# Kernel optimization log

Hardware: AMD Instinct MI355X
Metric: run time of the kernel (lower is better)

The kernel has to match this reference:

```python
import jax, jax.numpy as jnp
import numpy as np

ALPHA = 1.0          # gating temperature (train_alpha=False)
DEPTH = 4            # floor(log2(leaves=16))
LEAF_NUM = 16        # 2**DEPTH
N_INTERNAL = LEAF_NUM - 2  # nodes 1..14 (root handled separately)
B, D, OUT = 8192, 512, 64


def _prob(x, pw, aW, ab):
    # vectorized Node.prob with set_comps=True (comparators recomputed from batch mean)
    comp = -jnp.mean(x * pw, axis=0)                      # [in]
    dist = jax.nn.sigmoid(ALPHA * (pw * x + comp))        # [B, in]
    attn = jax.nn.softmax(x @ aW.T + ab, axis=-1)         # [B, in]
    return jnp.sum(dist * attn, axis=1, keepdims=True)    # [B, 1]


def setup_inputs() -> dict:
    key = jax.random.key(0)
    ks = jax.random.split(key, 12)
    s = 0.02
    return {
        "x": jax.random.normal(ks[0], (B, D), jnp.float32),
        # root node (input_size=D, output_size=D)
        "calc_W0": jax.random.normal(ks[1], (D, D), jnp.float32) * s,
        "calc_b0": jnp.zeros((D,), jnp.float32),
        "prob_w0": jax.random.uniform(ks[2], (D,), jnp.float32),
        "attn_W0": jax.random.normal(ks[3], (D, D), jnp.float32) * s,
        "attn_b0": jnp.zeros((D,), jnp.float32),
        # internal nodes 1..14 (input_size=2D, output_size=D), stacked
        "calc_W": jax.random.normal(ks[4], (N_INTERNAL, D, 2 * D), jnp.float32) * s,
        "calc_b": jnp.zeros((N_INTERNAL, D), jnp.float32),
        "prob_w": jax.random.uniform(ks[5], (N_INTERNAL, 2 * D), jnp.float32),
        "attn_W": jax.random.normal(ks[6], (N_INTERNAL, 2 * D, 2 * D), jnp.float32) * s,
        "attn_b": jnp.zeros((N_INTERNAL, 2 * D), jnp.float32),
        # leaf nodes: learned output vectors (torch.rand init)
        "leaf_out": jax.random.uniform(ks[7], (LEAF_NUM, OUT), jnp.float32),
    }


def reference(x, calc_W0, calc_b0, prob_w0, attn_W0, attn_b0,
              calc_W, calc_b, prob_w, attn_W, attn_b, leaf_out):
    outs, probab = {}, {}
    # root
    outs[0] = jax.nn.relu(x @ calc_W0.T + calc_b0)            # [B, D]
    p = _prob(x, prob_w0, attn_W0, attn_b0)                   # [B, 1]
    probab[1] = 1.0 - p
    probab[2] = p
    # internal nodes 1..leaf_num-2 (binary-tree routing)
    for n in range(1, LEAF_NUM - 1):
        parent = (n - 1) // 2
        inp = jnp.concatenate([outs[parent], x], axis=1)      # [B, 2D]
        outs[n] = jax.nn.relu(inp @ calc_W[n - 1].T + calc_b[n - 1])
        p = _prob(inp, prob_w[n - 1], attn_W[n - 1], attn_b[n - 1])
        probab[2 * n + 1] = probab[n] * (1.0 - p)
        probab[2 * n + 2] = probab[n] * p
    # leaves: indices LEAF_NUM-1 .. 2*LEAF_NUM-2
    leaf_p = jnp.concatenate([probab[i + LEAF_NUM - 1] for i in range(LEAF_NUM)], axis=1)  # [B, 16]
    # sum over leaves of probab * leaf_out == leaf_p @ leaf_out
    actions = leaf_p @ leaf_out                                # [B, OUT]
    return jax.nn.softmax(actions, axis=-1)
```

## Files before the change

### kernel.cpp

```cpp
#include <hip/hip_runtime.h>
#include <hip/hip_bf16.h>
#include <cstdint>


#define NROWS 8192
#define HALFD 512

typedef __bf16 bf16x8 __attribute__((ext_vector_type(8)));
typedef short  short8 __attribute__((ext_vector_type(8)));
typedef float  f32x4  __attribute__((ext_vector_type(4)));

union FragU { short8 s; bf16x8 b; };

struct GArgs {
  const __hip_bfloat16* A0[4];
  const __hip_bfloat16* Bw[4];
  const float* bias[4];
  const float* pw[4];
  const float* cm0[4];
  __hip_bfloat16* outB[4];
  float* csOut[4];
  float* S1[4];
  float* S2[4];
  int mode[4];
  int gx[4];
  int K[4];
};

__device__ __forceinline__ void gl2lds16(const void* g, void* l) {
  __builtin_amdgcn_global_load_lds((__attribute__((address_space(1))) void*)g,
                                   (__attribute__((address_space(3))) void*)l,
                                   16, 0, 0);
}

struct CvtArgs { const float* src[5]; __hip_bfloat16* dst[5]; int nblk[5]; };
__global__ void k_cvt(CvtArgs a) {
  int b = blockIdx.x, r = 0;
  while (b >= a.nblk[r]) { b -= a.nblk[r]; ++r; }
  const int i = (b * 256 + threadIdx.x) * 4;
  float4 v = *(const float4*)(a.src[r] + i);
  union { short4 s4; __hip_bfloat16 h[4]; } u;
  u.h[0] = __float2bfloat16(v.x);
  u.h[1] = __float2bfloat16(v.y);
  u.h[2] = __float2bfloat16(v.z);
  u.h[3] = __float2bfloat16(v.w);
  *(short4*)(a.dst[r] + i) = u.s4;
}

__global__ void k_colsum_f32(const float* __restrict__ src, float* __restrict__ dst) {
  int c  = blockIdx.x * 256 + threadIdx.x;
  int r0 = blockIdx.y * 256;
  float s = 0.f;
  for (int r = 0; r < 256; ++r) s += src[(size_t)(r0 + r) * HALFD + c];
  atomicAdd(&dst[c], s);
}

__global__ __launch_bounds__(512, 2)
void k_gemm(GArgs ga, const __hip_bfloat16* __restrict__ A1,
            const float* __restrict__ cm1) {
  __shared__ alignas(16) short As[2][256 * 64];
  __shared__ alignas(16) short Bs[2][256 * 64];

  const int z = blockIdx.z;
  const int id  = blockIdx.x + gridDim.x * blockIdx.y;
  const int xcd = id & 7;
  const int q   = id >> 3;
  const int bx  = q >> 2;
  const int by  = xcd * 4 + (q & 3);
  if (bx >= ga.gx[z]) return;

  const __hip_bfloat16* __restrict__ Ah0 = ga.A0[z];
  const __hip_bfloat16* __restrict__ Bw  = ga.Bw[z];
  const float* __restrict__ bias = ga.bias[z];
  const int K = ga.K[z];

  const int tid  = threadIdx.x;
  const int lane = tid & 63;
  const int wv   = tid >> 6;
  const int wm   = wv >> 2, wn = wv & 3;
  const int lr   = lane & 15, lg = lane >> 4;
  const int sw   = lr & 7;
  const int row0 = by * 256;
  const int col0 = bx * 256;

  f32x4 acc[8][4];
#pragma unroll
  for (int i = 0; i < 8; ++i)
#pragma unroll
    for (int j = 0; j < 4; ++j)
#pragma unroll
      for (int e = 0; e < 4; ++e) acc[i][j][e] = 0.f;

  const int sr  = tid >> 3;
  const int sc  = (((tid & 7) ^ (sr & 7)) << 3);
  const int wvB = wv * 1024;

#pragma unroll
  for (int rnd = 0; rnd < 4; ++rnd) {
    const int r = rnd * 64 + sr;
    gl2lds16(Ah0 + (size_t)(row0 + r) * HALFD + sc, (char*)As[0] + rnd * 8192 + wvB);
    gl2lds16(Bw  + (size_t)(col0 + r) * K + sc,     (char*)Bs[0] + rnd * 8192 + wvB);
  }
  __syncthreads();

  int cur = 0;
  for (int kt = 0; kt < K; kt += 64) {
    const int kn = kt + 64;
    if (kn < K) {
      const __hip_bfloat16* Asrc = (kn < HALFD) ? Ah0 : A1;
      const int kl = kn & (HALFD - 1);
#pragma unroll
      for (int rnd = 0; rnd < 4; ++rnd) {
        const int r = rnd * 64 + sr;
        gl2lds16(Asrc + (size_t)(row0 + r) * HALFD + kl + sc,
                 (char*)As[cur ^ 1] + rnd * 8192 + wvB);
        gl2lds16(Bw + (size_t)(col0 + r) * K + kn + sc,
                 (char*)Bs[cur ^ 1] + rnd * 8192 + wvB);
      }
    }
    const short* Ab = As[cur];
    const short* Bb = Bs[cur];
#pragma unroll
    for (int kk = 0; kk < 64; kk += 32) {
      FragU a[8], b[4];
#pragma unroll
      for (int mi = 0; mi < 8; ++mi)
        a[mi].s = *(const short8*)(Ab + (wm * 128 + mi * 16 + lr) * 64 +
                                   ((((kk >> 3) + lg) ^ sw) << 3));
#pragma unroll
      for (int ni = 0; ni < 4; ++ni)
        b[ni].s = *(const short8*)(Bb + (wn * 64 + ni * 16 + lr) * 64 +
                                   ((((kk >> 3) + lg) ^ sw) << 3));
#pragma unroll
      for (int mi = 0; mi < 8; ++mi)
#pragma unroll
        for (int ni = 0; ni < 4; ++ni)
          acc[mi][ni] = __builtin_amdgcn_mfma_f32_16x16x32_bf16(a[mi].b, b[ni].b,
                                                               acc[mi][ni], 0, 0, 0);
    }
    __syncthreads();
    cur ^= 1;
  }

  if (ga.mode[z] == 0) {
    __hip_bfloat16* outB = ga.outB[z];
    float* csOut = ga.csOut[z];
#pragma unroll
    for (int ni = 0; ni < 4; ++ni) {
      const int col  = col0 + wn * 64 + ni * 16 + lr;
      const float bv = bias[col];
      __hip_bfloat16* op = outB + (size_t)(col >> 9) * ((size_t)NROWS * HALFD) + (col & 511);
      float csum = 0.f;
#pragma unroll
      for (int mi = 0; mi < 8; ++mi) {
#pragma unroll
        for (int rg = 0; rg < 4; ++rg) {
          const int row = row0 + wm * 128 + mi * 16 + lg * 4 + rg;
          float v = acc[mi][ni][rg] + bv;
          v = v > 0.f ? v : 0.f;
          csum += v;
          op[(size_t)row * HALFD] = __float2bfloat16(v);
        }
      }
      csum += __shfl_xor(csum, 16);
      csum += __shfl_xor(csum, 32);
      if (lg == 0) atomicAdd(&csOut[col], csum);
    }
  } else {
    const float* __restrict__ pw  = ga.pw[z];
    const float* __restrict__ cm0 = ga.cm0[z];
    const int node  = col0 >> 10;
    const int slice = ((bx & 3) << 2) | wn;
    float* s1p = ga.S1[z] + (size_t)(node * 16 + slice) * NROWS;
    float* s2p = ga.S2[z] + (size_t)(node * 16 + slice) * NROWS;
    float bv[4], pwv[4], cmv[4];
    const __hip_bfloat16* Ain[4];
#pragma unroll
    for (int ni = 0; ni < 4; ++ni) {
      const int col = col0 + wn * 64 + ni * 16 + lr;
      bv[ni]  = bias[col];
      pwv[ni] = pw[col];
      const int ii   = col & 1023;
      const int half = ii >> 9;
      const int cc   = ii & 511;
      cmv[ni] = (half ? cm1[cc] : cm0[cc]) * (1.f / 8192.f);
      Ain[ni] = (half ? A1 : Ah0) + cc;
    }
#pragma unroll
    for (int mi = 0; mi < 8; ++mi) {
#pragma unroll
      for (int rg = 0; rg < 4; ++rg) {
        const int row = row0 + wm * 128 + mi * 16 + lg * 4 + rg;
        float s1 = 0.f, s2 = 0.f;
#pragma unroll
        for (int ni = 0; ni < 4; ++ni) {
          const float l = acc[mi][ni][rg] + bv[ni];
          const float e = __expf(l);
          const float inpv = __bfloat162float(Ain[ni][(size_t)row * HALFD]);
          const float zz = pwv[ni] * (inpv - cmv[ni]);
          const float dist = 1.f / (1.f + __expf(-zz));
          s1 += e;
          s2 += dist * e;
        }
#pragma unroll
        for (int off = 1; off < 16; off <<= 1) {
          s1 += __shfl_xor(s1, off);
          s2 += __shfl_xor(s2, off);
        }
        if (lr == 0) {
          s1p[row] = s1;
          s2p[row] = s2;
        }
      }
    }
  }
}

__global__ void k_finalize(const float* __restrict__ S1, const float* __restrict__ S2,
                           const float* __restrict__ leaf_out, float* __restrict__ out) {
  const int r    = (blockIdx.x * 256 + threadIdx.x) >> 6;
  const int lane = threadIdx.x & 63;
  float pb[31];
  pb[0] = 1.f;
#pragma unroll
  for (int n = 0; n < 15; ++n) {
    float a1 = 0.f, a2 = 0.f;
#pragma unroll
    for (int s = 0; s < 16; ++s) {
      a1 += S1[((size_t)n * 16 + s) * NROWS + r];
      a2 += S2[((size_t)n * 16 + s) * NROWS + r];
    }
    const float p = a2 / a1;
    pb[2 * n + 1] = pb[n] * (1.f - p);
    pb[2 * n + 2] = pb[n] * p;
  }
  float a = 0.f;
#pragma unroll
  for (int i = 0; i < 16; ++i) a += pb[15 + i] * leaf_out[i * 64 + lane];
  float m = a;
#pragma unroll
  for (int off = 1; off < 64; off <<= 1) m = fmaxf(m, __shfl_xor(m, off));
  const float e = __expf(a - m);
  float s = e;
#pragma unroll
  for (int off = 1; off < 64; off <<= 1) s += __shfl_xor(s, off);
  out[(size_t)r * 64 + lane] = e / s;
}

static constexpr size_t O_S1   = 0;
static constexpr size_t O_S2   = O_S1 + (size_t)15 * 16 * NROWS * 4;
static constexpr size_t O_XSUM = O_S2 + (size_t)15 * 16 * NROWS * 4;
static constexpr size_t O_CS   = O_XSUM + 512 * 4;
static constexpr size_t O_ZEND = O_CS + 7 * 512 * 4;
static constexpr size_t O_XB   = O_ZEND;
static constexpr size_t O_OUTS = O_XB + (size_t)NROWS * HALFD * 2;
static constexpr size_t O_CW0  = O_OUTS + 7 * (size_t)NROWS * HALFD * 2;
static constexpr size_t O_AW0  = O_CW0 + (size_t)512 * 512 * 2;
static constexpr size_t O_CW   = O_AW0 + (size_t)512 * 512 * 2;
static constexpr size_t O_AW   = O_CW + (size_t)14 * 512 * 1024 * 2;

extern "C" void kernel_launch(void* const* d_in, const int* in_sizes, int n_in,
                              void* d_out, int out_size, void* d_ws, size_t ws_size,
                              hipStream_t stream) {
  const float* x        = (const float*)d_in[0];
  const float* calc_b0  = (const float*)d_in[2];
  const float* prob_w0  = (const float*)d_in[3];
  const float* attn_b0  = (const float*)d_in[5];
  const float* calc_b   = (const float*)d_in[7];
  const float* prob_w   = (const float*)d_in[8];
  const float* attn_b   = (const float*)d_in[10];
  const float* leaf_out = (const float*)d_in[11];
  float* out = (float*)d_out;
  char* ws = (char*)d_ws;

  float* S1   = (float*)(ws + O_S1);
  float* S2   = (float*)(ws + O_S2);
  float* xsum = (float*)(ws + O_XSUM);
  float* cs   = (float*)(ws + O_CS);
  __hip_bfloat16* xb   = (__hip_bfloat16*)(ws + O_XB);
  __hip_bfloat16* outs = (__hip_bfloat16*)(ws + O_OUTS);
  __hip_bfloat16* cW0b = (__hip_bfloat16*)(ws + O_CW0);
  __hip_bfloat16* aW0b = (__hip_bfloat16*)(ws + O_AW0);
  __hip_bfloat16* cWb  = (__hip_bfloat16*)(ws + O_CW);
  __hip_bfloat16* aWb  = (__hip_bfloat16*)(ws + O_AW);
  const size_t OSZ = (size_t)NROWS * HALFD;
  const size_t NSL = (size_t)16 * NROWS;

  hipMemsetAsync(d_ws, 0, O_ZEND, stream);

  {
    CvtArgs ca{};
    ca.src[0] = x;                     ca.dst[0] = xb;   ca.nblk[0] = NROWS * HALFD / 1024;
    ca.src[1] = (const float*)d_in[1]; ca.dst[1] = cW0b; ca.nblk[1] = 512 * 512 / 1024;
    ca.src[2] = (const float*)d_in[4]; ca.dst[2] = aW0b; ca.nblk[2] = 512 * 512 / 1024;
    ca.src[3] = (const float*)d_in[6]; ca.dst[3] = cWb;  ca.nblk[3] = 14 * 512 * 1024 / 1024;
    ca.src[4] = (const float*)d_in[9]; ca.dst[4] = aWb;  ca.nblk[4] = 14 * 1024 * 1024 / 1024;
    int tot = ca.nblk[0] + ca.nblk[1] + ca.nblk[2] + ca.nblk[3] + ca.nblk[4];
    k_cvt<<<tot, 256, 0, stream>>>(ca);
  }
  k_colsum_f32<<<dim3(2, 32), 256, 0, stream>>>(x, xsum);

  {
    GArgs ga{};
    ga.mode[0] = 0; ga.gx[0] = 2; ga.K[0] = 512;
    ga.A0[0] = xb; ga.Bw[0] = cW0b; ga.bias[0] = calc_b0;
    ga.outB[0] = outs; ga.csOut[0] = cs;
    ga.mode[1] = 1; ga.gx[1] = 2; ga.K[1] = 512;
    ga.A0[1] = xb; ga.Bw[1] = aW0b; ga.bias[1] = attn_b0;
    ga.pw[1] = prob_w0; ga.cm0[1] = xsum;
    ga.S1[1] = S1; ga.S2[1] = S2;
    k_gemm<<<dim3(2, 32, 2), 512, 0, stream>>>(ga, xb, xsum);
  }
  {
    GArgs ga{};
    ga.mode[0] = 0; ga.gx[0] = 4; ga.K[0] = 1024;
    ga.A0[0] = outs; ga.Bw[0] = cWb; ga.bias[0] = calc_b;
    ga.outB[0] = outs + OSZ; ga.csOut[0] = cs + 512;
    ga.mode[1] = 1; ga.gx[1] = 8; ga.K[1] = 1024;
    ga.A0[1] = outs; ga.Bw[1] = aWb; ga.bias[1] = attn_b;
    ga.pw[1] = prob_w; ga.cm0[1] = cs;
    ga.S1[1] = S1 + (size_t)1 * NSL; ga.S2[1] = S2 + (size_t)1 * NSL;
    k_gemm<<<dim3(8, 32, 2), 512, 0, stream>>>(ga, xb, xsum);
  }
  {
    GArgs ga{};
    for (int i = 0; i < 2; ++i) {
      ga.mode[i] = 0; ga.gx[i] = 4; ga.K[i] = 1024;
      ga.A0[i] = outs + (size_t)(1 + i) * OSZ;
      ga.Bw[i] = cWb + (size_t)(2 + 2 * i) * 512 * 1024;
      ga.bias[i] = calc_b + (2 + 2 * i) * 512;
      ga.outB[i] = outs + (size_t)(3 + 2 * i) * OSZ;
      ga.csOut[i] = cs + (size_t)(3 + 2 * i) * 512;
    }
    for (int i = 0; i < 2; ++i) {
      const int zi = 2 + i;
      ga.mode[zi] = 1; ga.gx[zi] = 8; ga.K[zi] = 1024;
      ga.A0[zi] = outs + (size_t)(1 + i) * OSZ;
      ga.Bw[zi] = aWb + (size_t)(2 + 2 * i) * 1024 * 1024;
      ga.bias[zi] = attn_b + (2 + 2 * i) * 1024;
      ga.pw[zi] = prob_w + (2 + 2 * i) * 1024;
      ga.cm0[zi] = cs + (size_t)(1 + i) * 512;
      ga.S1[zi] = S1 + (size_t)(3 + 2 * i) * NSL;
      ga.S2[zi] = S2 + (size_t)(3 + 2 * i) * NSL;
    }
    k_gemm<<<dim3(8, 32, 4), 512, 0, stream>>>(ga, xb, xsum);
  }
  {
    GArgs ga{};
    for (int i = 0; i < 4; ++i) {
      ga.mode[i] = 1; ga.gx[i] = 8; ga.K[i] = 1024;
      ga.A0[i] = outs + (size_t)(3 + i) * OSZ;
      ga.Bw[i] = aWb + (size_t)(6 + 2 * i) * 1024 * 1024;
      ga.bias[i] = attn_b + (6 + 2 * i) * 1024;
      ga.pw[i] = prob_w + (6 + 2 * i) * 1024;
      ga.cm0[i] = cs + (size_t)(3 + i) * 512;
      ga.S1[i] = S1 + (size_t)(7 + 2 * i) * NSL;
      ga.S2[i] = S2 + (size_t)(7 + 2 * i) * NSL;
    }
    k_gemm<<<dim3(8, 32, 4), 512, 0, stream>>>(ga, xb, xsum);
  }

  k_finalize<<<NROWS * 64 / 256, 256, 0, stream>>>(S1, S2, leaf_out, out);
}
```

Before: 668.8 us.

## Restructure GEMM main loop into quadrant-staged 8-wave ping-pong pipeline

The GEMM K-loop is rewritten so each 256x256 tile is split into four 128x128 quadrants. Global-to-LDS loads for the next tile are issued per half between MFMA quadrant phases, with explicit vmcnt waits, raw s_barrier calls and s_setprio around the MFMA bursts. The goal is finer interleaving of memory traffic with matrix-core work than the single syncthreads double buffer allowed. The epilogues are remapped to the new quadrant accumulator layout. It carries risk in the hand-counted waitcnt values and the extra barriers.

Result: slower. 1.595 ms (+138.5%).

```diff
diff --git a/kernel.cpp b/kernel.cpp
--- a/kernel.cpp
+++ b/kernel.cpp
@@ -55,11 +55,74 @@
   atomicAdd(&dst[c], s);
 }
 
+
+#define LDA(BUF, H) do { \
+  _Pragma("unroll") for (int i_ = 0; i_ < 4; ++i_) \
+  _Pragma("unroll") for (int k_ = 0; k_ < 2; ++k_) \
+    a[i_][k_].s = *(const short8*)(&As[BUF][H][(wm * 64 + i_ * 16 + lr) * 64 + \
+                                   (((k_ * 4 + lg) ^ sw) << 3)]); \
+} while (0)
+
+#define LDB(BUF, H) do { \
+  _Pragma("unroll") for (int j_ = 0; j_ < 2; ++j_) \
+  _Pragma("unroll") for (int k_ = 0; k_ < 2; ++k_) \
+    b[j_][k_].s = *(const short8*)(&Bs[BUF][H][(wn * 32 + j_ * 16 + lr) * 64 + \
+                                   (((k_ * 4 + lg) ^ sw) << 3)]); \
+} while (0)
+
+#define MFMA_Q(MQ, NQ) do { \
+  _Pragma("unroll") for (int i_ = 0; i_ < 4; ++i_) \
+  _Pragma("unroll") for (int j_ = 0; j_ < 2; ++j_) \
+  _Pragma("unroll") for (int k_ = 0; k_ < 2; ++k_) \
+    acc[MQ][NQ][i_][j_] = __builtin_amdgcn_mfma_f32_16x16x32_bf16( \
+        a[i_][k_].b, b[j_][k_].b, acc[MQ][NQ][i_][j_], 0, 0, 0); \
+} while (0)
+
+#define STG_A(NB, H) do { \
+  gl2lds16(aS + (size_t)((H) * 128) * HALFD,      (char*)&As[NB][H][0] + wvB); \
+  gl2lds16(aS + (size_t)((H) * 128 + 64) * HALFD, (char*)&As[NB][H][0] + 8192 + wvB); \
+} while (0)
+
+#define STG_B(NB, H) do { \
+  gl2lds16(bS + (size_t)((H) * 128) * K,      (char*)&Bs[NB][H][0] + wvB); \
+  gl2lds16(bS + (size_t)((H) * 128 + 64) * K, (char*)&Bs[NB][H][0] + 8192 + wvB); \
+} while (0)
+
+#define TILE_BODY(BUF, NB, STG) do { \
+   \
+  if (STG) { STG_A(NB, 0); asm volatile("s_waitcnt vmcnt(6)" ::: "memory"); } \
+  else     { asm volatile("s_waitcnt vmcnt(4)" ::: "memory"); } \
+  __builtin_amdgcn_s_barrier(); \
+  LDA(BUF, 0); LDB(BUF, 0); \
+  __builtin_amdgcn_s_setprio(1); MFMA_Q(0, 0); __builtin_amdgcn_s_setprio(0); \
+  __builtin_amdgcn_s_barrier(); \
+   \
+  if (STG) { STG_B(NB, 0); asm volatile("s_waitcnt vmcnt(6)" ::: "memory"); } \
+  else     { asm volatile("s_waitcnt vmcnt(2)" ::: "memory"); } \
+  __builtin_amdgcn_s_barrier(); \
+  LDA(BUF, 1); \
+  __builtin_amdgcn_s_setprio(1); MFMA_Q(1, 0); __builtin_amdgcn_s_setprio(0); \
+  __builtin_amdgcn_s_barrier(); \
+   \
+  if (STG) { STG_A(NB, 1); asm volatile("s_waitcnt vmcnt(6)" ::: "memory"); } \
+  else     { asm volatile("s_waitcnt vmcnt(0)" ::: "memory"); } \
+  __builtin_amdgcn_s_barrier(); \
+  LDB(BUF, 1); \
+  __builtin_amdgcn_s_setprio(1); MFMA_Q(1, 1); __builtin_amdgcn_s_setprio(0); \
+  __builtin_amdgcn_s_barrier(); \
+   \
+  if (STG) { STG_B(NB, 1); } \
+  __builtin_amdgcn_s_barrier(); \
+  LDA(BUF, 0); \
+  __builtin_amdgcn_s_setprio(1); MFMA_Q(0, 1); __builtin_amdgcn_s_setprio(0); \
+  __builtin_amdgcn_s_barrier(); \
+} while (0)
+
 __global__ __launch_bounds__(512, 2)
 void k_gemm(GArgs ga, const __hip_bfloat16* __restrict__ A1,
             const float* __restrict__ cm1) {
-  __shared__ alignas(16) short As[2][256 * 64];
-  __shared__ alignas(16) short Bs[2][256 * 64];
+  __shared__ alignas(16) short As[2][2][128 * 64];
+  __shared__ alignas(16) short Bs[2][2][128 * 64];
 
   const int z = blockIdx.z;
   const int id  = blockIdx.x + gridDim.x * blockIdx.y;
@@ -72,7 +135,8 @@
   const __hip_bfloat16* __restrict__ Ah0 = ga.A0[z];
   const __hip_bfloat16* __restrict__ Bw  = ga.Bw[z];
   const float* __restrict__ bias = ga.bias[z];
-  const int K = ga.K[z];
+  const int K  = ga.K[z];
+  const int NT = K >> 6;
 
   const int tid  = threadIdx.x;
   const int lane = tid & 63;
@@ -80,91 +144,73 @@
   const int wm   = wv >> 2, wn = wv & 3;
   const int lr   = lane & 15, lg = lane >> 4;
   const int sw   = lr & 7;
+  const int wvB  = wv * 1024;
   const int row0 = by * 256;
   const int col0 = bx * 256;
 
-  f32x4 acc[8][4];
-#pragma unroll
-  for (int i = 0; i < 8; ++i)
-#pragma unroll
-    for (int j = 0; j < 4; ++j)
-#pragma unroll
-      for (int e = 0; e < 4; ++e) acc[i][j][e] = 0.f;
-
-  const int sr  = tid >> 3;
-  const int sc  = (((tid & 7) ^ (sr & 7)) << 3);
-  const int wvB = wv * 1024;
-
-#pragma unroll
-  for (int rnd = 0; rnd < 4; ++rnd) {
-    const int r = rnd * 64 + sr;
-    gl2lds16(Ah0 + (size_t)(row0 + r) * HALFD + sc, (char*)As[0] + rnd * 8192 + wvB);
-    gl2lds16(Bw  + (size_t)(col0 + r) * K + sc,     (char*)Bs[0] + rnd * 8192 + wvB);
-  }
-  __syncthreads();
-
-  int cur = 0;
-  for (int kt = 0; kt < K; kt += 64) {
-    const int kn = kt + 64;
-    if (kn < K) {
-      const __hip_bfloat16* Asrc = (kn < HALFD) ? Ah0 : A1;
-      const int kl = kn & (HALFD - 1);
-#pragma unroll
-      for (int rnd = 0; rnd < 4; ++rnd) {
-        const int r = rnd * 64 + sr;
-        gl2lds16(Asrc + (size_t)(row0 + r) * HALFD + kl + sc,
-                 (char*)As[cur ^ 1] + rnd * 8192 + wvB);
-        gl2lds16(Bw + (size_t)(col0 + r) * K + kn + sc,
-                 (char*)Bs[cur ^ 1] + rnd * 8192 + wvB);
-      }
-    }
-    const short* Ab = As[cur];
-    const short* Bb = Bs[cur];
-#pragma unroll
-    for (int kk = 0; kk < 64; kk += 32) {
-      FragU a[8], b[4];
-#pragma unroll
-      for (int mi = 0; mi < 8; ++mi)
-        a[mi].s = *(const short8*)(Ab + (wm * 128 + mi * 16 + lr) * 64 +
-                                   ((((kk >> 3) + lg) ^ sw) << 3));
-#pragma unroll
-      for (int ni = 0; ni < 4; ++ni)
-        b[ni].s = *(const short8*)(Bb + (wn * 64 + ni * 16 + lr) * 64 +
-                                   ((((kk >> 3) + lg) ^ sw) << 3));
-#pragma unroll
-      for (int mi = 0; mi < 8; ++mi)
-#pragma unroll
-        for (int ni = 0; ni < 4; ++ni)
-          acc[mi][ni] = __builtin_amdgcn_mfma_f32_16x16x32_bf16(a[mi].b, b[ni].b,
-                                                               acc[mi][ni], 0, 0, 0);
-    }
-    __syncthreads();
-    cur ^= 1;
+  f32x4 acc[2][2][4][2];
+#pragma unroll
+  for (int mq = 0; mq < 2; ++mq)
+#pragma unroll
+    for (int nq = 0; nq < 2; ++nq)
+#pragma unroll
+      for (int i = 0; i < 4; ++i)
+#pragma unroll
+        for (int j = 0; j < 2; ++j)
+#pragma unroll
+          for (int e = 0; e < 4; ++e) acc[mq][nq][i][j][e] = 0.f;
+
+  FragU a[4][2], b[2][2];
+
+  const int gc = (tid & 7) ^ ((tid >> 3) & 7);
+  const size_t aoff = (size_t)(row0 + (tid >> 3)) * HALFD + gc * 8;
+  const size_t boff = (size_t)(col0 + (tid >> 3)) * (size_t)K + gc * 8;
+
+  const __hip_bfloat16* aS = Ah0 + aoff;
+  const __hip_bfloat16* bS = Bw + boff;
+
+  STG_A(0, 0); STG_B(0, 0); STG_A(0, 1); STG_B(0, 1);
+
+  for (int T = 0; T < NT; ++T) {
+    const int sn  = T + 1;
+    const int stg = sn < NT;
+    if (stg) {
+      aS = ((sn < 8) ? Ah0 : A1) + ((sn & 7) << 6) + aoff;
+      bS = Bw + (size_t)sn * 64 + boff;
+    }
+    if (T & 1) TILE_BODY(1, 0, stg);
+    else       TILE_BODY(0, 1, stg);
   }
 
   if (ga.mode[z] == 0) {
     __hip_bfloat16* outB = ga.outB[z];
     float* csOut = ga.csOut[z];
 #pragma unroll
-    for (int ni = 0; ni < 4; ++ni) {
-      const int col  = col0 + wn * 64 + ni * 16 + lr;
-      const float bv = bias[col];
-      __hip_bfloat16* op = outB + (size_t)(col >> 9) * ((size_t)NROWS * HALFD) + (col & 511);
-      float csum = 0.f;
-#pragma unroll
-      for (int mi = 0; mi < 8; ++mi) {
-#pragma unroll
-        for (int rg = 0; rg < 4; ++rg) {
-          const int row = row0 + wm * 128 + mi * 16 + lg * 4 + rg;
-          float v = acc[mi][ni][rg] + bv;
-          v = v > 0.f ? v : 0.f;
-          csum += v;
-          op[(size_t)row * HALFD] = __float2bfloat16(v);
+    for (int nq = 0; nq < 2; ++nq) {
+#pragma unroll
+      for (int ni = 0; ni < 2; ++ni) {
+        const int col  = col0 + nq * 128 + wn * 32 + ni * 16 + lr;
+        const float bv = bias[col];
+        __hip_bfloat16* op = outB + (size_t)(col >> 9) * ((size_t)NROWS * HALFD) + (col & 511);
+        float csum = 0.f;
+#pragma unroll
+        for (int mq = 0; mq < 2; ++mq) {
+#pragma unroll
+          for (int mi = 0; mi < 4; ++mi) {
+#pragma unroll
+            for (int rg = 0; rg < 4; ++rg) {
+              const int row = row0 + mq * 128 + wm * 64 + mi * 16 + lg * 4 + rg;
+              float v = acc[mq][nq][mi][ni][rg] + bv;
+              v = v > 0.f ? v : 0.f;
+              csum += v;
+              op[(size_t)row * HALFD] = __float2bfloat16(v);
+            }
+          }
         }
+        csum += __shfl_xor(csum, 16);
+        csum += __shfl_xor(csum, 32);
+        if (lg == 0) atomicAdd(&csOut[col], csum);
       }
-      csum += __shfl_xor(csum, 16);
-      csum += __shfl_xor(csum, 32);
-      if (lg == 0) atomicAdd(&csOut[col], csum);
     }
   } else {
     const float* __restrict__ pw  = ga.pw[z];
@@ -173,43 +219,52 @@
     const int slice = ((bx & 3) << 2) | wn;
     float* s1p = ga.S1[z] + (size_t)(node * 16 + slice) * NROWS;
     float* s2p = ga.S2[z] + (size_t)(node * 16 + slice) * NROWS;
-    float bv[4], pwv[4], cmv[4];
-    const __hip_bfloat16* Ain[4];
-#pragma unroll
-    for (int ni = 0; ni < 4; ++ni) {
-      const int col = col0 + wn * 64 + ni * 16 + lr;
-      bv[ni]  = bias[col];
-      pwv[ni] = pw[col];
-      const int ii   = col & 1023;
-      const int half = ii >> 9;
-      const int cc   = ii & 511;
-      cmv[ni] = (half ? cm1[cc] : cm0[cc]) * (1.f / 8192.f);
-      Ain[ni] = (half ? A1 : Ah0) + cc;
-    }
-#pragma unroll
-    for (int mi = 0; mi < 8; ++mi) {
-#pragma unroll
-      for (int rg = 0; rg < 4; ++rg) {
-        const int row = row0 + wm * 128 + mi * 16 + lg * 4 + rg;
-        float s1 = 0.f, s2 = 0.f;
-#pragma unroll
-        for (int ni = 0; ni < 4; ++ni) {
-          const float l = acc[mi][ni][rg] + bv[ni];
-          const float e = __expf(l);
-          const float inpv = __bfloat162float(Ain[ni][(size_t)row * HALFD]);
-          const float zz = pwv[ni] * (inpv - cmv[ni]);
-          const float dist = 1.f / (1.f + __expf(-zz));
-          s1 += e;
-          s2 += dist * e;
-        }
-#pragma unroll
-        for (int off = 1; off < 16; off <<= 1) {
-          s1 += __shfl_xor(s1, off);
-          s2 += __shfl_xor(s2, off);
-        }
-        if (lr == 0) {
-          s1p[row] = s1;
-          s2p[row] = s2;
+    float bv[2][2], pwv[2][2], cmv[2][2];
+    const __hip_bfloat16* Ain[2][2];
+#pragma unroll
+    for (int nq = 0; nq < 2; ++nq) {
+#pragma unroll
+      for (int ni = 0; ni < 2; ++ni) {
+        const int col = col0 + nq * 128 + wn * 32 + ni * 16 + lr;
+        bv[nq][ni]  = bias[col];
+        pwv[nq][ni] = pw[col];
+        const int ii   = col & 1023;
+        const int half = ii >> 9;
+        const int cc   = ii & 511;
+        cmv[nq][ni] = (half ? cm1[cc] : cm0[cc]) * (1.f / 8192.f);
+        Ain[nq][ni] = (half ? A1 : Ah0) + cc;
+      }
+    }
+#pragma unroll
+    for (int mq = 0; mq < 2; ++mq) {
+#pragma unroll
+      for (int mi = 0; mi < 4; ++mi) {
+#pragma unroll
+        for (int rg = 0; rg < 4; ++rg) {
+          const int row = row0 + mq * 128 + wm * 64 + mi * 16 + lg * 4 + rg;
+          float s1 = 0.f, s2 = 0.f;
+#pragma unroll
+          for (int nq = 0; nq < 2; ++nq) {
+#pragma unroll
+            for (int ni = 0; ni < 2; ++ni) {
+              const float l = acc[mq][nq][mi][ni][rg] + bv[nq][ni];
+              const float e = __expf(l);
+              const float inpv = __bfloat162float(Ain[nq][ni][(size_t)row * HALFD]);
+              const float zz = pwv[nq][ni] * (inpv - cmv[nq][ni]);
+              const float dist = 1.f / (1.f + __expf(-zz));
+              s1 += e;
+              s2 += dist * e;
+            }
+          }
+#pragma unroll
+          for (int off = 1; off < 16; off <<= 1) {
+            s1 += __shfl_xor(s1, off);
+            s2 += __shfl_xor(s2, off);
+          }
+          if (lr == 0) {
+            s1p[row] = s1;
+            s2p[row] = s2;
+          }
         }
       }
     }
```
